# Optimization experiments

Measured on AMD Instinct MI355X. Metric: run time of the kernel, lower is better.

The kernel has to match this reference:

```python
import jax, jax.numpy as jnp
import numpy as np

D_MODEL = 2048
N_HEADS = 16
D_K = D_MODEL // N_HEADS
B = 2
S = 2048


def setup_inputs() -> dict:
    key = jax.random.key(0)
    ks = jax.random.split(key, 6)
    scale = 1.0 / np.sqrt(D_MODEL)
    return {
        "inp": jax.random.normal(ks[0], (B, S, D_MODEL), dtype=jnp.float32),
        "wq": jax.random.normal(ks[1], (D_MODEL, D_MODEL), dtype=jnp.float32) * scale,
        "wk": jax.random.normal(ks[2], (D_MODEL, D_MODEL), dtype=jnp.float32) * scale,
        "wv": jax.random.normal(ks[3], (D_MODEL, D_MODEL), dtype=jnp.float32) * scale,
        "wo": jax.random.normal(ks[4], (D_MODEL, D_MODEL), dtype=jnp.float32) * scale,
        "attn_bias": jax.random.normal(ks[5], (1, 1, S, S), dtype=jnp.float32),
        "softcap": 30,
    }


def reference(inp, wq, wk, wv, wo, attn_bias, softcap):
    # inp: [B, S, D]; weights stored torch-style [out, in] -> x @ W^T
    b, s, _ = inp.shape

    def split_heads(x):  # [B,S,D] -> [B,H,S,dk]
        return x.reshape(b, s, N_HEADS, D_K).transpose(0, 2, 1, 3)

    q = split_heads(inp @ wq.T)
    k = split_heads(inp @ wk.T)
    v = split_heads(inp @ wv.T)

    scale = 1.0 / np.sqrt(D_K).astype(np.float32)
    scores = jnp.einsum("bhqd,bhkd->bhqk", q, k) * scale + attn_bias
    cap = jnp.float32(softcap)
    scores = jnp.tanh(scores / cap) * cap  # softcap > 0 branch
    weights = jax.nn.softmax(scores, axis=-1)
    o = jnp.einsum("bhqk,bhkd->bhqd", weights, v)
    o = o.transpose(0, 2, 1, 3).reshape(b, s, D_MODEL)
    return o @ wo.T
```

## Files before the change

### kernel.cpp

```cpp
#include <hip/hip_runtime.h>

#define D_MODEL 2048
#define S_LEN 2048
#define NB 2
#define NH 16
#define DK 128

typedef __attribute__((ext_vector_type(8))) __bf16 bf16x8;
typedef __attribute__((ext_vector_type(4))) float f32x4;

__device__ __forceinline__ unsigned short f2bf(float f) {
    union { __bf16 b; unsigned short u; } cv;
    cv.b = (__bf16)f;
    return cv.u;
}

__device__ __forceinline__ void gld_lds16(const void* g, void* l) {
    __builtin_amdgcn_global_load_lds(
        (const __attribute__((address_space(1))) unsigned int*)g,
        (__attribute__((address_space(3))) unsigned int*)l, 16, 0, 0);
}

__global__ void cast_f32_to_bf16(const float* __restrict__ x,
                                 unsigned short* __restrict__ y, int n4) {
    int i = blockIdx.x * blockDim.x + threadIdx.x;
    int stride = gridDim.x * blockDim.x;
    const float4* x4 = (const float4*)x;
    ushort4* y4 = (ushort4*)y;
    for (; i < n4; i += stride) {
        float4 v = x4[i];
        ushort4 o;
        o.x = f2bf(v.x); o.y = f2bf(v.y); o.z = f2bf(v.z); o.w = f2bf(v.w);
        y4[i] = o;
    }
}

__global__ void cast4_f32_to_bf16(const float* __restrict__ x0, const float* __restrict__ x1,
                                  const float* __restrict__ x2, const float* __restrict__ x3,
                                  unsigned short* y0, unsigned short* y1,
                                  unsigned short* y2, unsigned short* y3, int n4) {
    const float* x = (blockIdx.y == 0) ? x0 : (blockIdx.y == 1) ? x1 : (blockIdx.y == 2) ? x2 : x3;
    unsigned short* y = (blockIdx.y == 0) ? y0 : (blockIdx.y == 1) ? y1 : (blockIdx.y == 2) ? y2 : y3;
    int i = blockIdx.x * blockDim.x + threadIdx.x;
    int stride = gridDim.x * blockDim.x;
    const float4* x4 = (const float4*)x;
    ushort4* y4 = (ushort4*)y;
    for (; i < n4; i += stride) {
        float4 v = x4[i];
        ushort4 o;
        o.x = f2bf(v.x); o.y = f2bf(v.y); o.z = f2bf(v.z); o.w = f2bf(v.w);
        y4[i] = o;
    }
}

#define BM 128
#define BN 128
#define BK 64

__device__ __forceinline__ void cstore(float* p, float v) { *p = v; }
__device__ __forceinline__ void cstore(unsigned short* p, float v) { *p = f2bf(v); }

template <typename OutT>
__global__ __launch_bounds__(256) void gemm_bt(const unsigned short* __restrict__ A,
                                               const unsigned short* __restrict__ Bt,
                                               OutT* __restrict__ C,
                                               int M, int N, int K) {
    __shared__ __align__(16) unsigned short As[BM * BK];
    __shared__ __align__(16) unsigned short Bs[BN * BK];
    const int tid = threadIdx.x;
    const int lane = tid & 63;
    const int wave = tid >> 6;
    const int quad = lane >> 4;
    const int l15 = lane & 15;
    const int wr = (wave >> 1) * 64;
    const int wc = (wave & 1) * 64;
    const int m0 = blockIdx.x * BM;
    const int n0 = blockIdx.y * BN;

    const int slotbase = wave * 64 + lane;

    f32x4 zero = {0.f, 0.f, 0.f, 0.f};
    f32x4 acc[4][4];
    for (int i = 0; i < 4; i++)
        for (int j = 0; j < 4; j++) acc[i][j] = zero;

    for (int k0 = 0; k0 < K; k0 += BK) {
        __syncthreads();
#pragma unroll
        for (int t = 0; t < 4; t++) {
            int slot = t * 256 + slotbase;
            int row = slot >> 3;
            int cg = (slot & 7) ^ (row & 7);
            gld_lds16(A + (size_t)(m0 + row) * K + k0 + cg * 8, &As[slot * 8]);
            gld_lds16(Bt + (size_t)(n0 + row) * K + k0 + cg * 8, &Bs[slot * 8]);
        }
        __syncthreads();

        bf16x8 af[4][2], bfr[4][2];
#pragma unroll
        for (int t = 0; t < 4; t++)
#pragma unroll
            for (int c = 0; c < 2; c++) {
                int ch = (c * 4 + quad) ^ (l15 & 7);
                af[t][c]  = *(const bf16x8*)(&As[((wr + t * 16 + l15) * 8 + ch) * 8]);
                bfr[t][c] = *(const bf16x8*)(&Bs[((wc + t * 16 + l15) * 8 + ch) * 8]);
            }
#pragma unroll
        for (int c = 0; c < 2; c++)
#pragma unroll
            for (int mt = 0; mt < 4; mt++)
#pragma unroll
                for (int nt = 0; nt < 4; nt++)
                    acc[mt][nt] = __builtin_amdgcn_mfma_f32_16x16x32_bf16(
                        af[mt][c], bfr[nt][c], acc[mt][nt], 0, 0, 0);
    }

#pragma unroll
    for (int mt = 0; mt < 4; mt++)
#pragma unroll
        for (int nt = 0; nt < 4; nt++)
#pragma unroll
            for (int r = 0; r < 4; r++) {
                int m = m0 + wr + mt * 16 + quad * 4 + r;
                int n = n0 + wc + nt * 16 + l15;
                cstore(&C[(size_t)m * N + n], acc[mt][nt][r]);
            }
}

#define QT 128
#define PS_STRIDE 72

__global__ __launch_bounds__(512, 4) void flash_attn(
        const unsigned short* __restrict__ Q,
        const unsigned short* __restrict__ K,
        const unsigned short* __restrict__ Vt,
        const float* __restrict__ bias,
        const int* __restrict__ softcap,
        unsigned short* __restrict__ O) {
    __shared__ __align__(16) unsigned short Ks[64 * DK];
    __shared__ __align__(16) unsigned short Vts[DK * 64];
    __shared__ __align__(16) unsigned short Ps[8 * 16 * PS_STRIDE];

    const int tid = threadIdx.x;
    const int lane = tid & 63;
    const int wave = tid >> 6;
    const int quad = lane >> 4;
    const int l15 = lane & 15;
    const int q0 = blockIdx.x * QT;
    const int h = blockIdx.y;
    const int b = blockIdx.z;

    const float scale = 0.08838834764831845f;
    const float cap = (float)softcap[0];
    const float LOG2E = 1.4426950408889634f;
    const float c1 = 2.0f * LOG2E * scale / cap;
    const float c2 = 2.0f * LOG2E / cap;
    const float c3 = -2.0f * cap * LOG2E;

    const size_t head_off = (size_t)b * S_LEN * D_MODEL + (size_t)h * DK;
    const size_t vt_row = (size_t)NB * S_LEN;
    const unsigned short* Vh = Vt + (size_t)h * DK * vt_row + (size_t)b * S_LEN;

    bf16x8 qf[4];
    {
        const unsigned short* Qp = Q + head_off + (size_t)(q0 + wave * 16 + l15) * D_MODEL;
#pragma unroll
        for (int c = 0; c < 4; c++)
            qf[c] = *(const bf16x8*)(Qp + c * 32 + quad * 8);
    }

    f32x4 zero = {0.f, 0.f, 0.f, 0.f};
    float l_part[4] = {0.f, 0.f, 0.f, 0.f};
    f32x4 o_acc[8];
#pragma unroll
    for (int d = 0; d < 8; d++) o_acc[d] = zero;

    unsigned short* Psw = &Ps[wave * 16 * PS_STRIDE];
    const int qrow = q0 + wave * 16 + quad * 4;

    for (int kt = 0; kt < S_LEN / 64; kt++) {
        const int kbase = kt * 64;
        __syncthreads();
#pragma unroll
        for (int t = 0; t < 2; t++) {
            int slot = t * 512 + tid;
            int kr = slot >> 4;
            int kc = (slot & 15) ^ (kr & 15);
            gld_lds16(K + head_off + (size_t)(kbase + kr) * D_MODEL + kc * 8,
                      &Ks[slot * 8]);
            int vr = slot >> 3;
            int vc = (slot & 7) ^ (vr & 7);
            gld_lds16(Vh + (size_t)vr * vt_row + kbase + vc * 8,
                      &Vts[slot * 8]);
        }
        __syncthreads();

        f32x4 s[4];
#pragma unroll
        for (int nt = 0; nt < 4; nt++) s[nt] = zero;
#pragma unroll
        for (int c = 0; c < 4; c++) {
            bf16x8 kf[4];
#pragma unroll
            for (int nt = 0; nt < 4; nt++)
                kf[nt] = *(const bf16x8*)(&Ks[((nt * 16 + l15) * 16 +
                                               ((c * 4 + quad) ^ l15)) * 8]);
#pragma unroll
            for (int nt = 0; nt < 4; nt++)
                s[nt] = __builtin_amdgcn_mfma_f32_16x16x32_bf16(qf[c], kf[nt], s[nt], 0, 0, 0);
        }

#pragma unroll
        for (int nt = 0; nt < 4; nt++) {
            const float* bp = bias + (size_t)qrow * S_LEN + kbase + nt * 16 + l15;
#pragma unroll
            for (int r = 0; r < 4; r++) {
                float arg = fmaf(s[nt][r], c1, bp[(size_t)r * S_LEN] * c2);
                float u = __builtin_amdgcn_exp2f(arg);
                float p = __builtin_amdgcn_exp2f(c3 * __builtin_amdgcn_rcpf(u + 1.0f));
                s[nt][r] = p;
                l_part[r] += p;
            }
        }

#pragma unroll
        for (int nt = 0; nt < 4; nt++)
#pragma unroll
            for (int r = 0; r < 4; r++)
                Psw[(quad * 4 + r) * PS_STRIDE + nt * 16 + l15] = f2bf(s[nt][r]);

#pragma unroll
        for (int c = 0; c < 2; c++) {
            bf16x8 pf = *(const bf16x8*)(&Psw[l15 * PS_STRIDE + c * 32 + quad * 8]);
#pragma unroll
            for (int dt = 0; dt < 8; dt++) {
                bf16x8 vf = *(const bf16x8*)(&Vts[((dt * 16 + l15) * 8 +
                                                   ((c * 4 + quad) ^ (l15 & 7))) * 8]);
                o_acc[dt] = __builtin_amdgcn_mfma_f32_16x16x32_bf16(pf, vf, o_acc[dt], 0, 0, 0);
            }
        }
    }

#pragma unroll
    for (int r = 0; r < 4; r++) {
        float l = l_part[r];
        l += __shfl_xor(l, 1, 64);
        l += __shfl_xor(l, 2, 64);
        l += __shfl_xor(l, 4, 64);
        l += __shfl_xor(l, 8, 64);
        float inv = 1.0f / l;
        int row = qrow + r;
        unsigned short* Op = O + (size_t)(b * S_LEN + row) * D_MODEL + h * DK;
#pragma unroll
        for (int dt = 0; dt < 8; dt++)
            Op[dt * 16 + l15] = f2bf(o_acc[dt][r] * inv);
    }
}

extern "C" void kernel_launch(void* const* d_in, const int* in_sizes, int n_in,
                              void* d_out, int out_size, void* d_ws, size_t ws_size,
                              hipStream_t stream) {
    const float* inp = (const float*)d_in[0];
    const float* wq  = (const float*)d_in[1];
    const float* wk  = (const float*)d_in[2];
    const float* wv  = (const float*)d_in[3];
    const float* wo  = (const float*)d_in[4];
    const float* bias = (const float*)d_in[5];
    const int* softcap = (const int*)d_in[6];
    float* out = (float*)d_out;

    unsigned short* ws = (unsigned short*)d_ws;
    const size_t n_inp = (size_t)NB * S_LEN * D_MODEL;
    const size_t n_w = (size_t)D_MODEL * D_MODEL;
    unsigned short* inp_b = ws;
    unsigned short* wq_b = inp_b + n_inp;
    unsigned short* wk_b = wq_b + n_w;
    unsigned short* wv_b = wk_b + n_w;
    unsigned short* wo_b = wv_b + n_w;
    unsigned short* Qb = wo_b + n_w;
    unsigned short* Kb = Qb + n_inp;
    unsigned short* Vtb = Kb + n_inp;
    unsigned short* Ob = Vtb + n_inp;

    cast_f32_to_bf16<<<dim3(1024), dim3(256), 0, stream>>>(inp, inp_b, (int)(n_inp / 4));
    cast4_f32_to_bf16<<<dim3(256, 4), dim3(256), 0, stream>>>(
        wq, wk, wv, wo, wq_b, wk_b, wv_b, wo_b, (int)(n_w / 4));

    dim3 gg(NB * S_LEN / BM, D_MODEL / BN);
    gemm_bt<unsigned short><<<gg, 256, 0, stream>>>(inp_b, wq_b, Qb, NB * S_LEN, D_MODEL, D_MODEL);
    gemm_bt<unsigned short><<<gg, 256, 0, stream>>>(inp_b, wk_b, Kb, NB * S_LEN, D_MODEL, D_MODEL);
    dim3 gv(D_MODEL / BM, NB * S_LEN / BN);
    gemm_bt<unsigned short><<<gv, 256, 0, stream>>>(wv_b, inp_b, Vtb, D_MODEL, NB * S_LEN, D_MODEL);

    flash_attn<<<dim3(S_LEN / QT, NH, NB), 512, 0, stream>>>(Qb, Kb, Vtb, bias, softcap, Ob);

    gemm_bt<float><<<gg, 256, 0, stream>>>(Ob, wo_b, out, NB * S_LEN, D_MODEL, D_MODEL);
}
```

Before: 449.5 us.

## Prefetch next K/V tiles during softmax in attention and merge Q/K projection GEMMs

```diff
diff --git a/kernel.cpp b/kernel.cpp
--- a/kernel.cpp
+++ b/kernel.cpp
@@ -61,10 +61,10 @@
 __device__ __forceinline__ void cstore(unsigned short* p, float v) { *p = f2bf(v); }
 
 template <typename OutT>
-__global__ __launch_bounds__(256) void gemm_bt(const unsigned short* __restrict__ A,
-                                               const unsigned short* __restrict__ Bt,
-                                               OutT* __restrict__ C,
-                                               int M, int N, int K) {
+__device__ __forceinline__ void gemm_body(const unsigned short* __restrict__ A,
+                                          const unsigned short* __restrict__ Bt,
+                                          OutT* __restrict__ C,
+                                          int M, int N, int K, int m0, int n0) {
     __shared__ __align__(16) unsigned short As[BM * BK];
     __shared__ __align__(16) unsigned short Bs[BN * BK];
     const int tid = threadIdx.x;
@@ -74,8 +74,6 @@
     const int l15 = lane & 15;
     const int wr = (wave >> 1) * 64;
     const int wc = (wave & 1) * 64;
-    const int m0 = blockIdx.x * BM;
-    const int n0 = blockIdx.y * BN;
 
     const int slotbase = wave * 64 + lane;
 
@@ -127,8 +125,29 @@
             }
 }
 
+template <typename OutT>
+__global__ __launch_bounds__(256) void gemm_bt(const unsigned short* __restrict__ A,
+                                               const unsigned short* __restrict__ Bt,
+                                               OutT* __restrict__ C,
+                                               int M, int N, int K) {
+    gemm_body(A, Bt, C, M, N, K, blockIdx.x * BM, blockIdx.y * BN);
+}
+
+__global__ __launch_bounds__(256) void gemm_qk(const unsigned short* __restrict__ A,
+                                               const unsigned short* __restrict__ Wq,
+                                               const unsigned short* __restrict__ Wk,
+                                               unsigned short* __restrict__ Qo,
+                                               unsigned short* __restrict__ Ko,
+                                               int M, int N, int K) {
+    const int sel = blockIdx.y >> 4;
+    const unsigned short* Bt = sel ? Wk : Wq;
+    unsigned short* C = sel ? Ko : Qo;
+    gemm_body(A, Bt, C, M, N, K, blockIdx.x * BM, (blockIdx.y & 15) * BN);
+}
+
 #define QT 128
 #define PS_STRIDE 72
+#define NT (S_LEN / 64)
 
 __global__ __launch_bounds__(512, 4) void flash_attn(
         const unsigned short* __restrict__ Q,
@@ -138,7 +157,7 @@
         const int* __restrict__ softcap,
         unsigned short* __restrict__ O) {
     __shared__ __align__(16) unsigned short Ks[64 * DK];
-    __shared__ __align__(16) unsigned short Vts[DK * 64];
+    __shared__ __align__(16) unsigned short Vts[2][DK * 64];
     __shared__ __align__(16) unsigned short Ps[8 * 16 * PS_STRIDE];
 
     const int tid = threadIdx.x;
@@ -178,9 +197,7 @@
     unsigned short* Psw = &Ps[wave * 16 * PS_STRIDE];
     const int qrow = q0 + wave * 16 + quad * 4;
 
-    for (int kt = 0; kt < S_LEN / 64; kt++) {
-        const int kbase = kt * 64;
-        __syncthreads();
+    auto stageK = [&](int kbase) {
 #pragma unroll
         for (int t = 0; t < 2; t++) {
             int slot = t * 512 + tid;
@@ -188,11 +205,24 @@
             int kc = (slot & 15) ^ (kr & 15);
             gld_lds16(K + head_off + (size_t)(kbase + kr) * D_MODEL + kc * 8,
                       &Ks[slot * 8]);
+        }
+    };
+    auto stageV = [&](int kbase, int buf) {
+#pragma unroll
+        for (int t = 0; t < 2; t++) {
+            int slot = t * 512 + tid;
             int vr = slot >> 3;
             int vc = (slot & 7) ^ (vr & 7);
             gld_lds16(Vh + (size_t)vr * vt_row + kbase + vc * 8,
-                      &Vts[slot * 8]);
-        }
+                      &Vts[buf][slot * 8]);
+        }
+    };
+
+    stageK(0);
+    stageV(0, 0);
+
+    for (int kt = 0; kt < NT; kt++) {
+        const int kbase = kt * 64;
         __syncthreads();
 
         f32x4 s[4];
@@ -210,12 +240,28 @@
                 s[nt] = __builtin_amdgcn_mfma_f32_16x16x32_bf16(qf[c], kf[nt], s[nt], 0, 0, 0);
         }
 
+        __syncthreads();
+
+        float bb[4][4];
 #pragma unroll
         for (int nt = 0; nt < 4; nt++) {
             const float* bp = bias + (size_t)qrow * S_LEN + kbase + nt * 16 + l15;
 #pragma unroll
+            for (int r = 0; r < 4; r++)
+                bb[nt][r] = bp[(size_t)r * S_LEN];
+        }
+        __builtin_amdgcn_sched_barrier(0);
+
+        if (kt + 1 < NT) {
+            stageK(kbase + 64);
+            stageV(kbase + 64, (kt + 1) & 1);
+        }
+
+#pragma unroll
+        for (int nt = 0; nt < 4; nt++) {
+#pragma unroll
             for (int r = 0; r < 4; r++) {
-                float arg = fmaf(s[nt][r], c1, bp[(size_t)r * S_LEN] * c2);
+                float arg = fmaf(s[nt][r], c1, bb[nt][r] * c2);
                 float u = __builtin_amdgcn_exp2f(arg);
                 float p = __builtin_amdgcn_exp2f(c3 * __builtin_amdgcn_rcpf(u + 1.0f));
                 s[nt][r] = p;
@@ -229,13 +275,14 @@
             for (int r = 0; r < 4; r++)
                 Psw[(quad * 4 + r) * PS_STRIDE + nt * 16 + l15] = f2bf(s[nt][r]);
 
+        const unsigned short* Vcur = Vts[kt & 1];
 #pragma unroll
         for (int c = 0; c < 2; c++) {
             bf16x8 pf = *(const bf16x8*)(&Psw[l15 * PS_STRIDE + c * 32 + quad * 8]);
 #pragma unroll
             for (int dt = 0; dt < 8; dt++) {
-                bf16x8 vf = *(const bf16x8*)(&Vts[((dt * 16 + l15) * 8 +
-                                                   ((c * 4 + quad) ^ (l15 & 7))) * 8]);
+                bf16x8 vf = *(const bf16x8*)(&Vcur[((dt * 16 + l15) * 8 +
+                                                    ((c * 4 + quad) ^ (l15 & 7))) * 8]);
                 o_acc[dt] = __builtin_amdgcn_mfma_f32_16x16x32_bf16(pf, vf, o_acc[dt], 0, 0, 0);
             }
         }
@@ -286,13 +333,13 @@
     cast4_f32_to_bf16<<<dim3(256, 4), dim3(256), 0, stream>>>(
         wq, wk, wv, wo, wq_b, wk_b, wv_b, wo_b, (int)(n_w / 4));
 
-    dim3 gg(NB * S_LEN / BM, D_MODEL / BN);
-    gemm_bt<unsigned short><<<gg, 256, 0, stream>>>(inp_b, wq_b, Qb, NB * S_LEN, D_MODEL, D_MODEL);
-    gemm_bt<unsigned short><<<gg, 256, 0, stream>>>(inp_b, wk_b, Kb, NB * S_LEN, D_MODEL, D_MODEL);
+    gemm_qk<<<dim3(NB * S_LEN / BM, 2 * D_MODEL / BN), 256, 0, stream>>>(
+        inp_b, wq_b, wk_b, Qb, Kb, NB * S_LEN, D_MODEL, D_MODEL);
     dim3 gv(D_MODEL / BM, NB * S_LEN / BN);
     gemm_bt<unsigned short><<<gv, 256, 0, stream>>>(wv_b, inp_b, Vtb, D_MODEL, NB * S_LEN, D_MODEL);
 
     flash_attn<<<dim3(S_LEN / QT, NH, NB), 512, 0, stream>>>(Qb, Kb, Vtb, bias, softcap, Ob);
 
+    dim3 gg(NB * S_LEN / BM, D_MODEL / BN);
     gemm_bt<float><<<gg, 256, 0, stream>>>(Ob, wo_b, out, NB * S_LEN, D_MODEL, D_MODEL);
 }
```

Measured after the change: 438.5 us. 2.5% less time.
